# Optimization experiments

Hardware: AMD Instinct MI355X
Metric: run time of the kernel (lower is better)

The kernel has to match this reference:

```python
import jax, jax.numpy as jnp
import numpy as np

DFAUD = 1024
DFRGB = 1024
DIM_K = 1024
N_HEADS = 4
B, T = 16, 1024


def setup_inputs() -> dict:
    key = jax.random.key(0)
    ks = jax.random.split(key, 11)
    s = lambda d: 1.0 / np.sqrt(d)
    return {
        "x": jax.random.normal(ks[0], (B, T, DFAUD), jnp.float32),
        "y": jax.random.normal(ks[1], (B, T, DFRGB), jnp.float32),
        "adj": jax.random.normal(ks[2], (B, T, T), jnp.float32),
        "Wq": jax.random.uniform(ks[3], (DIM_K, DFAUD), jnp.float32, -s(DFAUD), s(DFAUD)),
        "bq": jnp.zeros((DIM_K,), jnp.float32),
        "Wk": jax.random.uniform(ks[4], (DIM_K, DFRGB), jnp.float32, -s(DFRGB), s(DFRGB)),
        "bk": jnp.zeros((DIM_K,), jnp.float32),
        "Wv": jax.random.uniform(ks[5], (DIM_K, DFRGB), jnp.float32, -s(DFRGB), s(DFRGB)),
        "bv": jnp.zeros((DIM_K,), jnp.float32),
        "Wo": jax.random.uniform(ks[6], (DFRGB, DIM_K), jnp.float32, -s(DIM_K), s(DIM_K)),
        "bo": jnp.zeros((DFRGB,), jnp.float32),
    }


def reference(x, y, adj, Wq, bq, Wk, bk, Wv, bv, Wo, bo):
    b, t = x.shape[0], x.shape[1]
    dh = DIM_K // N_HEADS
    norm = 1.0 / np.sqrt(DIM_K)
    # Faithful reproduction of the torch reshape(-1, B, T, dim_k // n_heads):
    # [B, T, dim_k] -> [n_heads, B, T, dh] (row-major reshape, layout-mixing for h>1)
    Q = (x @ Wq.T + bq).reshape(N_HEADS, b, t, dh)
    K = (y @ Wk.T + bk).reshape(N_HEADS, b, t, dh)
    V = (y @ Wv.T + bv).reshape(N_HEADS, b, t, dh)
    scores = jnp.einsum('hbqd,hbkd->hbqk', Q, K) * norm  # [h, B, T, T]
    att = jax.nn.softmax(scores + adj, axis=-1)          # adj [B,T,T] broadcasts
    temp = jnp.einsum('hbqk,hbkd->hbqd', att, V).reshape(b, t, DIM_K)
    out = (temp @ Wo.T + bo).reshape(-1, t, y.shape[2])
    return out
```

## Files before the change

### kernel.cpp

```cpp
#include <hip/hip_runtime.h>
#include <stdint.h>
#include <string.h>

typedef unsigned short u16;
typedef __attribute__((ext_vector_type(8))) short short8_t;
typedef __attribute__((ext_vector_type(4))) float f32x4;

typedef const __attribute__((address_space(1))) void GV;
typedef __attribute__((address_space(3))) void LV;

__device__ __forceinline__ void gload_lds16(const void* g, void* l) {
  __builtin_amdgcn_global_load_lds((GV*)g, (LV*)l, 16, 0, 0);
}

__device__ __forceinline__ u16 f2bf(float f) {
  union { float f; uint32_t u; } v; v.f = f;
  return (u16)((v.u + 0x7FFFu + ((v.u >> 16) & 1u)) >> 16);
}

__device__ __forceinline__ f32x4 fz4() { f32x4 v = {0.f, 0.f, 0.f, 0.f}; return v; }

__global__ __launch_bounds__(256) void cast_all(const float* __restrict__ x,
                                                const float* __restrict__ y,
                                                const float* __restrict__ w0,
                                                const float* __restrict__ w1,
                                                const float* __restrict__ w2,
                                                const float* __restrict__ w3,
                                                u16* __restrict__ xo,
                                                u16* __restrict__ yo,
                                                u16* __restrict__ o0,
                                                u16* __restrict__ o1,
                                                u16* __restrict__ o2,
                                                u16* __restrict__ o3) {
  const int bid = blockIdx.x;
  const float* in;
  u16* out;
  int off;
  if (bid < 32768) {
    in = (bid < 16384) ? x : y;
    out = (bid < 16384) ? xo : yo;
    off = bid & 16383;
  } else {
    const int s = (bid - 32768) >> 10;
    in = s == 0 ? w0 : s == 1 ? w1 : s == 2 ? w2 : w3;
    out = s == 0 ? o0 : s == 1 ? o1 : s == 2 ? o2 : o3;
    off = (bid - 32768) & 1023;
  }
  int i = (off * 256 + threadIdx.x) * 4;
  float4 v = *(const float4*)(in + i);
  ushort4 o;
  o.x = f2bf(v.x); o.y = f2bf(v.y); o.z = f2bf(v.z); o.w = f2bf(v.w);
  *(ushort4*)(out + i) = o;
}

template <int MODE>
__device__ __forceinline__ void gemm8_core(int bid, const u16* __restrict__ A,
                                           const u16* __restrict__ B,
                                           const float* __restrict__ bias,
                                           void* __restrict__ Cout,
                                           u16* Al, u16* Bl) {
  const int N = 1024, K = 1024;
  const int tid = threadIdx.x, w = tid >> 6, l = tid & 63;
  const int g = l >> 4, q = l & 15;
  const int xcd = bid & 7;
  const int nt = (bid >> 3) & 3;
  const int mt = xcd * 8 + (bid >> 5);
  const int n0 = nt * 256, m0 = mt * 256;
  const int NT = K >> 6;
  const int ah = w >> 2;
  const int bh = (w & 3) >> 1;
  const int brow0 = ((w & 3) & 1) * 64;

#define BROW(u)                                                                   \
  (MODE == 2 ? ((((u) >> 4) & 3) * 256 + nt * 64 + (((u) >> 6) & 3) * 16 + ((u) & 15)) \
             : (n0 + (((u) & 0xC0) | (((u) & 15) << 2) | (((u) >> 4) & 3))))

#define STAGE_A(S, half)                                                          \
  {                                                                               \
    _Pragma("unroll") for (int j_ = 0; j_ < 2; ++j_) {                            \
      const int idx_ = j_ * 512 + tid;                                            \
      const int row_ = idx_ >> 3;                                                 \
      const int sl_ = (idx_ & 7) ^ (((idx_ >> 5) & 1) << 1);                      \
      gload_lds16(A + (size_t)(m0 + (half) * 128 + row_) * K + (S) * 64 + sl_ * 8,\
                  Al + ((S) & 1) * 16384 + (half) * 8192 + (j_ * 512 + w * 64) * 8);\
    }                                                                             \
  }
#define STAGE_B(S, half)                                                          \
  {                                                                               \
    _Pragma("unroll") for (int j_ = 0; j_ < 2; ++j_) {                            \
      const int idx_ = j_ * 512 + tid;                                            \
      const int row_ = idx_ >> 3;                                                 \
      const int sl_ = (idx_ & 7) ^ (((idx_ >> 5) & 1) << 1);                      \
      const int pr_ = BROW((half) * 128 + row_);                                  \
      gload_lds16(B + (size_t)pr_ * K + (S) * 64 + sl_ * 8,                       \
                  Bl + ((S) & 1) * 16384 + (half) * 8192 + (j_ * 512 + w * 64) * 8);\
    }                                                                             \
  }

  f32x4 acc[8][4];
#pragma unroll
  for (int i = 0; i < 8; ++i)
#pragma unroll
    for (int n = 0; n < 4; ++n) acc[i][n] = fz4();

  const int wc = (w & 3) * 64;
  float bv[4];
#pragma unroll
  for (int nf = 0; nf < 4; ++nf) bv[nf] = bias[BROW(wc + nf * 16 + q)];

  STAGE_A(0, 0); STAGE_A(0, 1); STAGE_B(0, 0); STAGE_B(0, 1);
  STAGE_A(1, 0); STAGE_A(1, 1); STAGE_B(1, 0); STAGE_B(1, 1);
  asm volatile("s_waitcnt vmcnt(8)");
  __builtin_amdgcn_s_barrier();

  short8_t bfr[4][2];
  for (int S = 0; S < NT; ++S) {
    const int bs = (S & 1) * 16384;
#pragma unroll
    for (int p = 0; p < 4; ++p) {
      short8_t afr[2][2];
#pragma unroll
      for (int mi = 0; mi < 2; ++mi)
#pragma unroll
        for (int kk = 0; kk < 2; ++kk) {
          const int r = (2 * p + mi) * 16 + q;
          afr[mi][kk] = *(const short8_t*)(Al + bs + ah * 8192 + r * 64 +
                                           ((kk * 4 + g) ^ (((r >> 2) & 1) << 1)) * 8);
        }
      if (p == 0) {
#pragma unroll
        for (int nf = 0; nf < 4; ++nf)
#pragma unroll
          for (int kk = 0; kk < 2; ++kk) {
            const int r = brow0 + nf * 16 + q;
            bfr[nf][kk] = *(const short8_t*)(Bl + bs + bh * 8192 + r * 64 +
                                             ((kk * 4 + g) ^ (((r >> 2) & 1) << 1)) * 8);
          }
      }
      if (p == 0 && S >= 1 && S + 1 < NT) STAGE_A(S + 1, 0);
      if (p == 1 && S >= 1 && S + 1 < NT) STAGE_A(S + 1, 1);
      if (p == 2 && S + 2 < NT) STAGE_B(S + 2, 0);
      if (p == 3 && S + 2 < NT) STAGE_B(S + 2, 1);
      if (p == 3) {
        if (S == NT - 2) { asm volatile("s_waitcnt vmcnt(0)"); }
        else if (S < NT - 2) { asm volatile("s_waitcnt vmcnt(4)"); }
      }
      __builtin_amdgcn_s_barrier();
      asm volatile("s_waitcnt lgkmcnt(0)" ::: "memory");
      __builtin_amdgcn_sched_barrier(0);
      __builtin_amdgcn_s_setprio(1);
#pragma unroll
      for (int nf = 0; nf < 4; ++nf)
#pragma unroll
        for (int mi = 0; mi < 2; ++mi)
#pragma unroll
          for (int kk = 0; kk < 2; ++kk)
            acc[2 * p + mi][nf] = __builtin_amdgcn_mfma_f32_16x16x32_bf16(
                afr[mi][kk], bfr[nf][kk], acc[2 * p + mi][nf], 0, 0, 0);
      __builtin_amdgcn_s_setprio(0);
      __builtin_amdgcn_s_barrier();
    }
  }
#undef STAGE_A
#undef STAGE_B
#undef BROW

  const int wr = (w >> 2) * 128;
  if (MODE == 2) {
    const int dvt = nt * 64 + (w & 3) * 16 + q;
#pragma unroll
    for (int mf = 0; mf < 8; ++mf) {
#pragma unroll
      for (int j = 0; j < 4; ++j) {
        const int row = m0 + wr + mf * 16 + g * 4 + j;
        ushort4 st;
        st.x = f2bf(acc[mf][0][j] + bv[0]);
        st.y = f2bf(acc[mf][1][j] + bv[1]);
        st.z = f2bf(acc[mf][2][j] + bv[2]);
        st.w = f2bf(acc[mf][3][j] + bv[3]);
        *(ushort4*)((u16*)Cout + (((size_t)(row >> 8)) << 18) +
                    (((size_t)dvt) << 10) + ((row & 255) << 2)) = st;
      }
    }
  } else {
    const int colb = n0 + wc + q * 4;
#pragma unroll
    for (int mf = 0; mf < 8; ++mf) {
#pragma unroll
      for (int j = 0; j < 4; ++j) {
        const int row = m0 + wr + mf * 16 + g * 4 + j;
        if (MODE == 0) {
          float4 fv;
          fv.x = acc[mf][0][j] + bv[0];
          fv.y = acc[mf][1][j] + bv[1];
          fv.z = acc[mf][2][j] + bv[2];
          fv.w = acc[mf][3][j] + bv[3];
          *(float4*)((float*)Cout + (size_t)row * N + colb) = fv;
        } else {
          ushort4 st;
          st.x = f2bf(acc[mf][0][j] + bv[0]);
          st.y = f2bf(acc[mf][1][j] + bv[1]);
          st.z = f2bf(acc[mf][2][j] + bv[2]);
          st.w = f2bf(acc[mf][3][j] + bv[3]);
          *(ushort4*)((u16*)Cout + (size_t)row * N + colb) = st;
        }
      }
    }
  }
}

__global__ __launch_bounds__(512, 2) void gemm8_qkv(const u16* __restrict__ Xb,
                                                    const u16* __restrict__ Yb,
                                                    const u16* __restrict__ Wqb,
                                                    const u16* __restrict__ Wkb,
                                                    const u16* __restrict__ Wvb,
                                                    const float* __restrict__ bq,
                                                    const float* __restrict__ bk,
                                                    const float* __restrict__ bv,
                                                    u16* __restrict__ Qb,
                                                    u16* __restrict__ Kb,
                                                    u16* __restrict__ VTb) {
  __shared__ u16 Al[2 * 16384];
  __shared__ u16 Bl[2 * 16384];
  const int sel = blockIdx.x >> 8, bid = blockIdx.x & 255;
  if (sel == 0)      gemm8_core<1>(bid, Xb, Wqb, bq, Qb, Al, Bl);
  else if (sel == 1) gemm8_core<1>(bid, Yb, Wkb, bk, Kb, Al, Bl);
  else               gemm8_core<2>(bid, Yb, Wvb, bv, VTb, Al, Bl);
}

__global__ __launch_bounds__(512, 2) void gemm8_out(const u16* __restrict__ A,
                                                    const u16* __restrict__ B,
                                                    const float* __restrict__ bias,
                                                    float* __restrict__ C) {
  __shared__ u16 Al[2 * 16384];
  __shared__ u16 Bl[2 * 16384];
  gemm8_core<0>(blockIdx.x, A, B, bias, C, Al, Bl);
}

__global__ __launch_bounds__(256) void attn_kernel(const u16* __restrict__ Q,
                                                   const u16* __restrict__ Kf,
                                                   const u16* __restrict__ VT,
                                                   const float* __restrict__ adj,
                                                   u16* __restrict__ O) {
  __shared__ u16 Ks[32 * 256];
  __shared__ u16 Vs[256 * 32];
  const int tid = threadIdx.x, w = tid >> 6, l = tid & 63;
  const int g = l >> 4, q = l & 15;
  const int bid = blockIdx.x;
  const int xcd = bid & 7, idx = bid >> 3;
  const int b = xcd * 2 + (idx >> 6);
  const int qb = (idx >> 2) & 15, h = idx & 3;
  const int hb = h * 16 + b;
  const int q0 = qb * 64;
  const u16* qb_p = Q + ((size_t)hb * 1024 + q0 + w * 16) * 256;
  const u16* kb = Kf + (size_t)hb * 1024 * 256;
  const u16* vtb = VT + (size_t)hb * 256 * 1024;
  const float* adjr = adj + (size_t)b * 1024 * 1024 + (size_t)(q0 + w * 16 + q) * 1024;

  const int krow_b = tid >> 5;
  const int kslot = tid & 31;
  const int vdr_b = tid >> 2;
  const int vsl = tid & 3;

  short8_t qf[8];
#pragma unroll
  for (int kk = 0; kk < 8; ++kk)
    qf[kk] = *(const short8_t*)(qb_p + (size_t)q * 256 + kk * 32 + g * 8);

  f32x4 o[16];
#pragma unroll
  for (int n = 0; n < 16; ++n) o[n] = fz4();
  float mrun = -1e30f, lrun = 0.f;

  short8_t kst[4], vst[4];

#define LOADREGS(ktt)                                                              \
  {                                                                                \
    _Pragma("unroll") for (int i_ = 0; i_ < 4; ++i_) {                             \
      const int row_ = i_ * 8 + krow_b;                                            \
      kst[i_] = *(const short8_t*)(kb + (size_t)((ktt) * 32 + row_) * 256 +        \
                                   kslot * 8);                                     \
    }                                                                              \
    _Pragma("unroll") for (int i_ = 0; i_ < 4; ++i_) {                             \
      const int dr_ = i_ * 64 + vdr_b;                                             \
      vst[i_] = *(const short8_t*)(vtb + (size_t)dr_ * 1024 + (ktt) * 32 +         \
                                   vsl * 8);                                       \
    }                                                                              \
  }
#define WRITEREGS()                                                                \
  {                                                                                \
    _Pragma("unroll") for (int i_ = 0; i_ < 4; ++i_) {                             \
      const int row_ = i_ * 8 + krow_b;                                            \
      *(short8_t*)((char*)Ks + row_ * 512 + ((kslot ^ (row_ & 7)) * 16)) = kst[i_];\
    }                                                                              \
    _Pragma("unroll") for (int i_ = 0; i_ < 4; ++i_) {                             \
      const int dr_ = i_ * 64 + vdr_b;                                             \
      *(short8_t*)((char*)Vs + dr_ * 64 + ((vsl ^ ((dr_ >> 1) & 3)) * 16)) = vst[i_];\
    }                                                                              \
  }

  LOADREGS(0);
  float4 a0 = *(const float4*)(adjr + 0 * 32 + 0 * 16 + g * 4);
  float4 a1 = *(const float4*)(adjr + 0 * 32 + 1 * 16 + g * 4);
  WRITEREGS();
  __syncthreads();

  for (int kt = 0; kt < 32; ++kt) {
    float4 n0v = a0, n1v = a1;
    if (kt < 31) {
      LOADREGS(kt + 1);
      n0v = *(const float4*)(adjr + (kt + 1) * 32 + 0 * 16 + g * 4);
      n1v = *(const float4*)(adjr + (kt + 1) * 32 + 1 * 16 + g * 4);
    }

    f32x4 s[2];
    __builtin_amdgcn_s_setprio(1);
#pragma unroll
    for (int f = 0; f < 2; ++f) {
      f32x4 a = fz4();
      const int row = f * 16 + q;
      const char* kr = (const char*)Ks + row * 512;
#pragma unroll
      for (int kk = 0; kk < 8; ++kk) {
        const int cb = kk * 64 + g * 16;
        short8_t kfr = *(const short8_t*)(kr + (cb ^ ((row & 7) << 4)));
        a = __builtin_amdgcn_mfma_f32_16x16x32_bf16(kfr, qf[kk], a, 0, 0, 0);
      }
      s[f] = a;
    }
    __builtin_amdgcn_s_setprio(0);

#pragma unroll
    for (int j = 0; j < 4; ++j) {
      s[0][j] = s[0][j] * 0.03125f + ((const float*)&a0)[j];
      s[1][j] = s[1][j] * 0.03125f + ((const float*)&a1)[j];
    }

    float pmax = s[0][0];
#pragma unroll
    for (int j = 1; j < 4; ++j) pmax = fmaxf(pmax, s[0][j]);
#pragma unroll
    for (int j = 0; j < 4; ++j) pmax = fmaxf(pmax, s[1][j]);
    pmax = fmaxf(pmax, __shfl_xor(pmax, 16));
    pmax = fmaxf(pmax, __shfl_xor(pmax, 32));

    if (!__all(pmax - mrun <= 8.0f)) {
      const float mn = fmaxf(mrun, pmax);
      const float al = __expf(mrun - mn);
      mrun = mn;
      lrun *= al;
#pragma unroll
      for (int n = 0; n < 16; ++n)
#pragma unroll
        for (int r = 0; r < 4; ++r) o[n][r] *= al;
    }

    float sum = 0.f;
#pragma unroll
    for (int f = 0; f < 2; ++f)
#pragma unroll
      for (int j = 0; j < 4; ++j) {
        const float p = __expf(s[f][j] - mrun);
        s[f][j] = p;
        sum += p;
      }
    sum += __shfl_xor(sum, 16);
    sum += __shfl_xor(sum, 32);
    lrun += sum;

    uint32_t W00, W01, W10, W11;
    asm("v_cvt_pk_bf16_f32 %0, %1, %2" : "=v"(W00) : "v"(s[0][0]), "v"(s[0][1]));
    asm("v_cvt_pk_bf16_f32 %0, %1, %2" : "=v"(W01) : "v"(s[0][2]), "v"(s[0][3]));
    asm("v_cvt_pk_bf16_f32 %0, %1, %2" : "=v"(W10) : "v"(s[1][0]), "v"(s[1][1]));
    asm("v_cvt_pk_bf16_f32 %0, %1, %2" : "=v"(W11) : "v"(s[1][2]), "v"(s[1][3]));
    const uint32_t sA0 = (g < 2) ? W00 : W10;
    const uint32_t sA1 = (g < 2) ? W01 : W11;
    const uint32_t sB0 = (g < 2) ? W10 : W00;
    const uint32_t sB1 = (g < 2) ? W11 : W01;
    const uint32_t A0 = (uint32_t)__shfl_xor((int)sA0, 16);
    const uint32_t A1 = (uint32_t)__shfl_xor((int)sA1, 16);
    const uint32_t B0 = (uint32_t)__shfl_xor((int)sB0, 32);
    const uint32_t B1 = (uint32_t)__shfl_xor((int)sB1, 32);
    const uint32_t C0 = (uint32_t)__shfl_xor((int)sB0, 48);
    const uint32_t C1 = (uint32_t)__shfl_xor((int)sB1, 48);
    union { uint32_t u[4]; short8_t v; } pu;
    pu.u[0] = (g == 0) ? W00 : (g == 1) ? C0 : (g == 2) ? B0 : A0;
    pu.u[1] = (g == 0) ? W01 : (g == 1) ? C1 : (g == 2) ? B1 : A1;
    pu.u[2] = (g == 0) ? A0 : (g == 1) ? B0 : (g == 2) ? C0 : W10;
    pu.u[3] = (g == 0) ? A1 : (g == 1) ? B1 : (g == 2) ? C1 : W11;
    const short8_t pa = pu.v;

    __builtin_amdgcn_s_setprio(1);
#pragma unroll
    for (int n = 0; n < 16; ++n) {
      const int dr = n * 16 + q;
      const int sl = g ^ ((dr >> 1) & 3);
      short8_t vf = *(const short8_t*)((const char*)Vs + dr * 64 + sl * 16);
      o[n] = __builtin_amdgcn_mfma_f32_16x16x32_bf16(vf, pa, o[n], 0, 0, 0);
    }
    __builtin_amdgcn_s_setprio(0);

    if (kt < 31) {
      __syncthreads();
      WRITEREGS();
      __syncthreads();
    }
    a0 = n0v; a1 = n1v;
  }
#undef LOADREGS
#undef WRITEREGS

  const float inv = 1.0f / lrun;
  u16* ob = O + ((size_t)hb * 1024 + q0 + w * 16 + q) * 256;
#pragma unroll
  for (int n = 0; n < 16; ++n) {
    ushort4 st;
    st.x = f2bf(o[n][0] * inv); st.y = f2bf(o[n][1] * inv);
    st.z = f2bf(o[n][2] * inv); st.w = f2bf(o[n][3] * inv);
    *(ushort4*)(ob + n * 16 + g * 4) = st;
  }
}

extern "C" void kernel_launch(void* const* d_in, const int* in_sizes, int n_in,
                              void* d_out, int out_size, void* d_ws, size_t ws_size,
                              hipStream_t stream) {
  (void)in_sizes; (void)n_in; (void)out_size; (void)ws_size;
  const float* x   = (const float*)d_in[0];
  const float* y   = (const float*)d_in[1];
  const float* adj = (const float*)d_in[2];
  const float* Wq  = (const float*)d_in[3];
  const float* bq  = (const float*)d_in[4];
  const float* Wk  = (const float*)d_in[5];
  const float* bk  = (const float*)d_in[6];
  const float* Wv  = (const float*)d_in[7];
  const float* bv  = (const float*)d_in[8];
  const float* Wo  = (const float*)d_in[9];
  const float* bo  = (const float*)d_in[10];

  char* ws = (char*)d_ws;
  const size_t MB = 1ull << 20;
  u16* Xb  = (u16*)(ws + 0);
  u16* Yb  = (u16*)(ws + 32 * MB);
  u16* Wqb = (u16*)(ws + 64 * MB);
  u16* Wkb = (u16*)(ws + 66 * MB);
  u16* Wvb = (u16*)(ws + 68 * MB);
  u16* Wob = (u16*)(ws + 70 * MB);
  u16* Qb  = (u16*)(ws + 72 * MB);
  u16* Kb  = (u16*)(ws + 104 * MB);
  u16* VTb = (u16*)(ws + 168 * MB);
  u16* Tmp = Xb;

  cast_all<<<36864, 256, 0, stream>>>(x, y, Wq, Wk, Wv, Wo,
                                      Xb, Yb, Wqb, Wkb, Wvb, Wob);

  gemm8_qkv<<<768, 512, 0, stream>>>(Xb, Yb, Wqb, Wkb, Wvb, bq, bk, bv, Qb, Kb, VTb);

  attn_kernel<<<1024, 256, 0, stream>>>(Qb, Kb, VTb, adj, Tmp);

  gemm8_out<<<256, 512, 0, stream>>>(Tmp, Wob, bo, (float*)d_out);
}
```

Baseline: 332.3 us.

## Switch GEMM core to K-step 32 with halved LDS and two-phase MFMA

Rewrites the shared GEMM core used by the QKV and output projections to step K by 32 instead of 64. LDS buffers shrink by half, the XOR swizzle changes to a 4-slot pattern, and each K step is split into two MFMA halves over A rows. The next A tile and next B tile are issued between those halves, with a full vmcnt(0) wait each step. This lowers LDS footprint and register pressure, which may let more blocks share a CU. The cost is twice as many iterations and barriers, plus less prefetch depth from the full wait.

```diff
diff --git a/kernel.cpp b/kernel.cpp
--- a/kernel.cpp
+++ b/kernel.cpp
@@ -54,11 +54,11 @@
 }
 
 template <int MODE>
-__device__ __forceinline__ void gemm8_core(int bid, const u16* __restrict__ A,
-                                           const u16* __restrict__ B,
-                                           const float* __restrict__ bias,
-                                           void* __restrict__ Cout,
-                                           u16* Al, u16* Bl) {
+__device__ __forceinline__ void gemm32_core(int bid, const u16* __restrict__ A,
+                                            const u16* __restrict__ B,
+                                            const float* __restrict__ bias,
+                                            void* __restrict__ Cout,
+                                            u16* Al, u16* Bl) {
   const int N = 1024, K = 1024;
   const int tid = threadIdx.x, w = tid >> 6, l = tid & 63;
   const int g = l >> 4, q = l & 15;
@@ -66,34 +66,30 @@
   const int nt = (bid >> 3) & 3;
   const int mt = xcd * 8 + (bid >> 5);
   const int n0 = nt * 256, m0 = mt * 256;
-  const int NT = K >> 6;
-  const int ah = w >> 2;
-  const int bh = (w & 3) >> 1;
-  const int brow0 = ((w & 3) & 1) * 64;
+  const int NT = K >> 5;
 
 #define BROW(u)                                                                   \
   (MODE == 2 ? ((((u) >> 4) & 3) * 256 + nt * 64 + (((u) >> 6) & 3) * 16 + ((u) & 15)) \
              : (n0 + (((u) & 0xC0) | (((u) & 15) << 2) | (((u) >> 4) & 3))))
 
-#define STAGE_A(S, half)                                                          \
+#define STAGE_A32(S)                                                              \
   {                                                                               \
-    _Pragma("unroll") for (int j_ = 0; j_ < 2; ++j_) {                            \
-      const int idx_ = j_ * 512 + tid;                                            \
-      const int row_ = idx_ >> 3;                                                 \
-      const int sl_ = (idx_ & 7) ^ (((idx_ >> 5) & 1) << 1);                      \
-      gload_lds16(A + (size_t)(m0 + (half) * 128 + row_) * K + (S) * 64 + sl_ * 8,\
-                  Al + ((S) & 1) * 16384 + (half) * 8192 + (j_ * 512 + w * 64) * 8);\
+    _Pragma("unroll") for (int i_ = 0; i_ < 2; ++i_) {                            \
+      const int idx_ = i_ * 512 + tid;                                            \
+      const int row_ = idx_ >> 2;                                                 \
+      const int sl_ = (idx_ & 3) ^ (row_ & 3);                                    \
+      gload_lds16(A + (size_t)(m0 + row_) * K + (S) * 32 + sl_ * 8,               \
+                  Al + ((S) & 1) * 8192 + (i_ * 512 + w * 64) * 8);               \
     }                                                                             \
   }
-#define STAGE_B(S, half)                                                          \
+#define STAGE_B32(S)                                                              \
   {                                                                               \
-    _Pragma("unroll") for (int j_ = 0; j_ < 2; ++j_) {                            \
-      const int idx_ = j_ * 512 + tid;                                            \
-      const int row_ = idx_ >> 3;                                                 \
-      const int sl_ = (idx_ & 7) ^ (((idx_ >> 5) & 1) << 1);                      \
-      const int pr_ = BROW((half) * 128 + row_);                                  \
-      gload_lds16(B + (size_t)pr_ * K + (S) * 64 + sl_ * 8,                       \
-                  Bl + ((S) & 1) * 16384 + (half) * 8192 + (j_ * 512 + w * 64) * 8);\
+    _Pragma("unroll") for (int i_ = 0; i_ < 2; ++i_) {                            \
+      const int idx_ = i_ * 512 + tid;                                            \
+      const int row_ = idx_ >> 2;                                                 \
+      const int sl_ = (idx_ & 3) ^ (row_ & 3);                                    \
+      gload_lds16(B + (size_t)BROW(row_) * K + (S) * 32 + sl_ * 8,                \
+                  Bl + ((S) & 1) * 8192 + (i_ * 512 + w * 64) * 8);               \
     }                                                                             \
   }
 
@@ -108,61 +104,63 @@
 #pragma unroll
   for (int nf = 0; nf < 4; ++nf) bv[nf] = bias[BROW(wc + nf * 16 + q)];
 
-  STAGE_A(0, 0); STAGE_A(0, 1); STAGE_B(0, 0); STAGE_B(0, 1);
-  STAGE_A(1, 0); STAGE_A(1, 1); STAGE_B(1, 0); STAGE_B(1, 1);
-  asm volatile("s_waitcnt vmcnt(8)");
+  STAGE_A32(0); STAGE_B32(0); STAGE_A32(1); STAGE_B32(1);
+  asm volatile("s_waitcnt vmcnt(4)");
   __builtin_amdgcn_s_barrier();
 
-  short8_t bfr[4][2];
+  const int arow0 = (w >> 2) * 128 + q;
+  const int brow0 = (w & 3) * 64 + q;
   for (int S = 0; S < NT; ++S) {
-    const int bs = (S & 1) * 16384;
-#pragma unroll
-    for (int p = 0; p < 4; ++p) {
-      short8_t afr[2][2];
-#pragma unroll
-      for (int mi = 0; mi < 2; ++mi)
-#pragma unroll
-        for (int kk = 0; kk < 2; ++kk) {
-          const int r = (2 * p + mi) * 16 + q;
-          afr[mi][kk] = *(const short8_t*)(Al + bs + ah * 8192 + r * 64 +
-                                           ((kk * 4 + g) ^ (((r >> 2) & 1) << 1)) * 8);
-        }
-      if (p == 0) {
-#pragma unroll
-        for (int nf = 0; nf < 4; ++nf)
-#pragma unroll
-          for (int kk = 0; kk < 2; ++kk) {
-            const int r = brow0 + nf * 16 + q;
-            bfr[nf][kk] = *(const short8_t*)(Bl + bs + bh * 8192 + r * 64 +
-                                             ((kk * 4 + g) ^ (((r >> 2) & 1) << 1)) * 8);
-          }
-      }
-      if (p == 0 && S >= 1 && S + 1 < NT) STAGE_A(S + 1, 0);
-      if (p == 1 && S >= 1 && S + 1 < NT) STAGE_A(S + 1, 1);
-      if (p == 2 && S + 2 < NT) STAGE_B(S + 2, 0);
-      if (p == 3 && S + 2 < NT) STAGE_B(S + 2, 1);
-      if (p == 3) {
-        if (S == NT - 2) { asm volatile("s_waitcnt vmcnt(0)"); }
-        else if (S < NT - 2) { asm volatile("s_waitcnt vmcnt(4)"); }
-      }
-      __builtin_amdgcn_s_barrier();
-      asm volatile("s_waitcnt lgkmcnt(0)" ::: "memory");
-      __builtin_amdgcn_sched_barrier(0);
-      __builtin_amdgcn_s_setprio(1);
-#pragma unroll
-      for (int nf = 0; nf < 4; ++nf)
-#pragma unroll
-        for (int mi = 0; mi < 2; ++mi)
-#pragma unroll
-          for (int kk = 0; kk < 2; ++kk)
-            acc[2 * p + mi][nf] = __builtin_amdgcn_mfma_f32_16x16x32_bf16(
-                afr[mi][kk], bfr[nf][kk], acc[2 * p + mi][nf], 0, 0, 0);
-      __builtin_amdgcn_s_setprio(0);
-      __builtin_amdgcn_s_barrier();
-    }
-  }
-#undef STAGE_A
-#undef STAGE_B
+    const int bs = (S & 1) * 8192;
+    short8_t bfr[4], afr[4];
+#pragma unroll
+    for (int nf = 0; nf < 4; ++nf) {
+      const int r = brow0 + nf * 16;
+      bfr[nf] = *(const short8_t*)(Bl + bs + r * 32 + ((g ^ (r & 3)) * 8));
+    }
+#pragma unroll
+    for (int mf = 0; mf < 4; ++mf) {
+      const int r = arow0 + mf * 16;
+      afr[mf] = *(const short8_t*)(Al + bs + r * 32 + ((g ^ (r & 3)) * 8));
+    }
+    if (S >= 1 && S + 1 < NT) STAGE_A32(S + 1);
+    __builtin_amdgcn_s_barrier();
+    asm volatile("s_waitcnt lgkmcnt(0)" ::: "memory");
+    __builtin_amdgcn_sched_barrier(0);
+    __builtin_amdgcn_s_setprio(1);
+#pragma unroll
+    for (int nf = 0; nf < 4; ++nf)
+#pragma unroll
+      for (int mf = 0; mf < 4; ++mf)
+        acc[mf][nf] = __builtin_amdgcn_mfma_f32_16x16x32_bf16(afr[mf], bfr[nf],
+                                                              acc[mf][nf], 0, 0, 0);
+    __builtin_amdgcn_s_setprio(0);
+    __builtin_amdgcn_s_barrier();
+
+    short8_t afr2[4];
+#pragma unroll
+    for (int mf = 0; mf < 4; ++mf) {
+      const int r = arow0 + (4 + mf) * 16;
+      afr2[mf] = *(const short8_t*)(Al + bs + r * 32 + ((g ^ (r & 3)) * 8));
+    }
+    if (S >= 1 && S + 1 < NT) STAGE_B32(S + 1);
+    if (S + 1 < NT) { asm volatile("s_waitcnt vmcnt(0)"); }
+    __builtin_amdgcn_s_barrier();
+    asm volatile("s_waitcnt lgkmcnt(0)" ::: "memory");
+    __builtin_amdgcn_sched_barrier(0);
+    __builtin_amdgcn_s_setprio(1);
+#pragma unroll
+    for (int nf = 0; nf < 4; ++nf)
+#pragma unroll
+      for (int mf = 0; mf < 4; ++mf)
+        acc[4 + mf][nf] = __builtin_amdgcn_mfma_f32_16x16x32_bf16(afr2[mf], bfr[nf],
+                                                                  acc[4 + mf][nf],
+                                                                  0, 0, 0);
+    __builtin_amdgcn_s_setprio(0);
+    __builtin_amdgcn_s_barrier();
+  }
+#undef STAGE_A32
+#undef STAGE_B32
 #undef BROW
 
   const int wr = (w >> 2) * 128;
@@ -220,21 +218,21 @@
                                                     u16* __restrict__ Qb,
                                                     u16* __restrict__ Kb,
                                                     u16* __restrict__ VTb) {
-  __shared__ u16 Al[2 * 16384];
-  __shared__ u16 Bl[2 * 16384];
+  __shared__ u16 Al[2 * 8192];
+  __shared__ u16 Bl[2 * 8192];
   const int sel = blockIdx.x >> 8, bid = blockIdx.x & 255;
-  if (sel == 0)      gemm8_core<1>(bid, Xb, Wqb, bq, Qb, Al, Bl);
-  else if (sel == 1) gemm8_core<1>(bid, Yb, Wkb, bk, Kb, Al, Bl);
-  else               gemm8_core<2>(bid, Yb, Wvb, bv, VTb, Al, Bl);
+  if (sel == 0)      gemm32_core<1>(bid, Xb, Wqb, bq, Qb, Al, Bl);
+  else if (sel == 1) gemm32_core<1>(bid, Yb, Wkb, bk, Kb, Al, Bl);
+  else               gemm32_core<2>(bid, Yb, Wvb, bv, VTb, Al, Bl);
 }
 
 __global__ __launch_bounds__(512, 2) void gemm8_out(const u16* __restrict__ A,
                                                     const u16* __restrict__ B,
                                                     const float* __restrict__ bias,
                                                     float* __restrict__ C) {
-  __shared__ u16 Al[2 * 16384];
-  __shared__ u16 Bl[2 * 16384];
-  gemm8_core<0>(blockIdx.x, A, B, bias, C, Al, Bl);
+  __shared__ u16 Al[2 * 8192];
+  __shared__ u16 Bl[2 * 8192];
+  gemm32_core<0>(blockIdx.x, A, B, bias, C, Al, Bl);
 }
 
 __global__ __launch_bounds__(256) void attn_kernel(const u16* __restrict__ Q,
```

Measured after the change: 335.6 us. No clear change (+1.0%).

## Load K fragments directly from global into registers, bypassing LDS

Applied to the files above, without the earlier changes.

The attention kernel no longer stages K tiles through shared memory. Each wave loads its own K MFMA fragments straight from global memory into 16 registers, prefetched one tile ahead, while V still goes through LDS. The QK^T products are split across four independent accumulators to shorten the MFMA dependency chains. This removes the K LDS writes and reads at the cost of about 64 extra VGPRs and each of the four waves re-reading the same K tile from global memory or L2.

```diff
diff --git a/kernel.cpp b/kernel.cpp
--- a/kernel.cpp
+++ b/kernel.cpp
@@ -242,7 +242,6 @@
                                                    const u16* __restrict__ VT,
                                                    const float* __restrict__ adj,
                                                    u16* __restrict__ O) {
-  __shared__ u16 Ks[32 * 256];
   __shared__ u16 Vs[256 * 32];
   const int tid = threadIdx.x, w = tid >> 6, l = tid & 63;
   const int g = l >> 4, q = l & 15;
@@ -257,8 +256,6 @@
   const u16* vtb = VT + (size_t)hb * 256 * 1024;
   const float* adjr = adj + (size_t)b * 1024 * 1024 + (size_t)(q0 + w * 16 + q) * 1024;
 
-  const int krow_b = tid >> 5;
-  const int kslot = tid & 31;
   const int vdr_b = tid >> 2;
   const int vsl = tid & 3;
 
@@ -272,63 +269,63 @@
   for (int n = 0; n < 16; ++n) o[n] = fz4();
   float mrun = -1e30f, lrun = 0.f;
 
-  short8_t kst[4], vst[4];
-
-#define LOADREGS(ktt)                                                              \
+  short8_t kfr[16];
+  short8_t vst[4];
+
+#define LOADK(ktt)                                                                 \
   {                                                                                \
-    _Pragma("unroll") for (int i_ = 0; i_ < 4; ++i_) {                             \
-      const int row_ = i_ * 8 + krow_b;                                            \
-      kst[i_] = *(const short8_t*)(kb + (size_t)((ktt) * 32 + row_) * 256 +        \
-                                   kslot * 8);                                     \
-    }                                                                              \
+    _Pragma("unroll") for (int f_ = 0; f_ < 2; ++f_)                               \
+    _Pragma("unroll") for (int kk_ = 0; kk_ < 8; ++kk_)                            \
+      kfr[f_ * 8 + kk_] = *(const short8_t*)(kb +                                  \
+          (size_t)((ktt) * 32 + f_ * 16 + q) * 256 + kk_ * 32 + g * 8);            \
+  }
+#define LOADV(ktt)                                                                 \
+  {                                                                                \
     _Pragma("unroll") for (int i_ = 0; i_ < 4; ++i_) {                             \
       const int dr_ = i_ * 64 + vdr_b;                                             \
       vst[i_] = *(const short8_t*)(vtb + (size_t)dr_ * 1024 + (ktt) * 32 +         \
                                    vsl * 8);                                       \
     }                                                                              \
   }
-#define WRITEREGS()                                                                \
+#define WRITEV()                                                                   \
   {                                                                                \
-    _Pragma("unroll") for (int i_ = 0; i_ < 4; ++i_) {                             \
-      const int row_ = i_ * 8 + krow_b;                                            \
-      *(short8_t*)((char*)Ks + row_ * 512 + ((kslot ^ (row_ & 7)) * 16)) = kst[i_];\
-    }                                                                              \
     _Pragma("unroll") for (int i_ = 0; i_ < 4; ++i_) {                             \
       const int dr_ = i_ * 64 + vdr_b;                                             \
       *(short8_t*)((char*)Vs + dr_ * 64 + ((vsl ^ ((dr_ >> 1) & 3)) * 16)) = vst[i_];\
     }                                                                              \
   }
 
-  LOADREGS(0);
+  LOADK(0);
+  LOADV(0);
   float4 a0 = *(const float4*)(adjr + 0 * 32 + 0 * 16 + g * 4);
   float4 a1 = *(const float4*)(adjr + 0 * 32 + 1 * 16 + g * 4);
-  WRITEREGS();
+  WRITEV();
   __syncthreads();
 
   for (int kt = 0; kt < 32; ++kt) {
+    f32x4 s[2];
+    {
+      f32x4 c00 = fz4(), c01 = fz4(), c10 = fz4(), c11 = fz4();
+      __builtin_amdgcn_s_setprio(1);
+#pragma unroll
+      for (int kk = 0; kk < 4; ++kk) {
+        c00 = __builtin_amdgcn_mfma_f32_16x16x32_bf16(kfr[kk], qf[kk], c00, 0, 0, 0);
+        c01 = __builtin_amdgcn_mfma_f32_16x16x32_bf16(kfr[kk + 4], qf[kk + 4], c01, 0, 0, 0);
+        c10 = __builtin_amdgcn_mfma_f32_16x16x32_bf16(kfr[8 + kk], qf[kk], c10, 0, 0, 0);
+        c11 = __builtin_amdgcn_mfma_f32_16x16x32_bf16(kfr[12 + kk], qf[kk + 4], c11, 0, 0, 0);
+      }
+      __builtin_amdgcn_s_setprio(0);
+      s[0] = c00 + c01;
+      s[1] = c10 + c11;
+    }
+
     float4 n0v = a0, n1v = a1;
     if (kt < 31) {
-      LOADREGS(kt + 1);
+      LOADK(kt + 1);
+      LOADV(kt + 1);
       n0v = *(const float4*)(adjr + (kt + 1) * 32 + 0 * 16 + g * 4);
       n1v = *(const float4*)(adjr + (kt + 1) * 32 + 1 * 16 + g * 4);
     }
-
-    f32x4 s[2];
-    __builtin_amdgcn_s_setprio(1);
-#pragma unroll
-    for (int f = 0; f < 2; ++f) {
-      f32x4 a = fz4();
-      const int row = f * 16 + q;
-      const char* kr = (const char*)Ks + row * 512;
-#pragma unroll
-      for (int kk = 0; kk < 8; ++kk) {
-        const int cb = kk * 64 + g * 16;
-        short8_t kfr = *(const short8_t*)(kr + (cb ^ ((row & 7) << 4)));
-        a = __builtin_amdgcn_mfma_f32_16x16x32_bf16(kfr, qf[kk], a, 0, 0, 0);
-      }
-      s[f] = a;
-    }
-    __builtin_amdgcn_s_setprio(0);
 
 #pragma unroll
     for (int j = 0; j < 4; ++j) {
@@ -402,13 +399,14 @@
 
     if (kt < 31) {
       __syncthreads();
-      WRITEREGS();
+      WRITEV();
       __syncthreads();
     }
     a0 = n0v; a1 = n1v;
   }
-#undef LOADREGS
-#undef WRITEREGS
+#undef LOADK
+#undef LOADV
+#undef WRITEV
 
   const float inv = 1.0f / lrun;
   u16* ob = O + ((size_t)hb * 1024 + q0 + w * 16 + q) * 256;
```

After: 548.6 us. +65.1%, slower.
